# Kernel tuning notes

Measured on AMD Instinct MI355X. Metric: run time of the kernel, lower is better.

## Reference

```python
import jax, jax.numpy as jnp
import numpy as np
import itertools

RADIUS = 0.1
DILATION = 0.05
KSIZE = 3
NDIM = 3
EPS = 1e-12


def _offsets():
    # 3^ndim kernel-cell offsets centered on the particle, spaced by dilation
    half = (KSIZE - 1) / 2.0
    offs = np.array(list(itertools.product(range(KSIZE), repeat=NDIM)), dtype=np.float32)
    return jnp.asarray((offs - half) * DILATION)  # [K, NDIM]


def setup_inputs() -> dict:
    key = jax.random.key(0)
    k1, k2, k3, k4, k5 = jax.random.split(key, 5)
    B, N, C, O = 2, 4096, 16, 16
    K = KSIZE ** NDIM
    locs = jax.random.uniform(k1, (B, N, NDIM), dtype=jnp.float32)
    data = jax.random.normal(k2, (B, N, C), dtype=jnp.float32)
    # densities strictly positive, bounded away from zero
    density = jax.random.uniform(k3, (B, N), dtype=jnp.float32, minval=0.5, maxval=1.5)
    weight = jax.random.normal(k4, (O, C, K), dtype=jnp.float32) * 0.1
    bias = jax.random.normal(k5, (O,), dtype=jnp.float32) * 0.01
    return {"locs": locs, "data": data, "density": density, "weight": weight, "bias": bias}


def reference(locs, data, density, weight, bias):
    # SPH continuous convolution (ConvSP):
    # out[b,i,o] = bias[o] + sum_k sum_c weight[o,c,k] *
    #              sum_j (data[b,j,c]/density[b,j]) * W(||locs[b,j] - (locs[b,i]+off_k)||)
    # with smoothing kernel W(d) = (1 - d/radius)^3 for d < radius, else 0.
    B, N, _ = locs.shape
    O = weight.shape[0]
    offs = _offsets()                                # [K, NDIM]
    wK = jnp.transpose(weight, (2, 0, 1))            # [K, O, C]
    nd = data / density[..., None]                   # [B, N, C] density-normalized features
    l2 = jnp.sum(locs * locs, axis=-1)               # [B, N]

    def step(acc, xs):
        off, wk = xs                                 # off:[NDIM], wk:[O,C]
        c = locs + off                               # shifted query centers [B,N,NDIM]
        c2 = jnp.sum(c * c, axis=-1)                 # [B,N]
        d2 = c2[:, :, None] + l2[:, None, :] - 2.0 * jnp.einsum('bid,bjd->bij', c, locs)
        d = jnp.sqrt(jnp.maximum(d2, EPS))           # [B,N,N]
        w = jnp.where(d < RADIUS, (1.0 - d / RADIUS) ** 3, 0.0)
        kv = jnp.einsum('bij,bjc->bic', w, nd)       # [B,N,C]
        return acc + jnp.einsum('bic,oc->bio', kv, wk), None

    init = jnp.zeros((B, N, O), dtype=data.dtype)
    out, _ = jax.lax.scan(jax.checkpoint(step), init, (offs, wK))
    return out + bias
```

## Files before the change

kernel.cpp:

```cpp
#include <hip/hip_runtime.h>

#define NP 4096
#define NSLAB 64
#define ZSPAN 10
#define EPS_K 1e-12f
#define MAXH 256

__global__ __launch_bounds__(1024) void k_bins(const float* __restrict__ locs,
                                               int* __restrict__ off,
                                               int* __restrict__ cursor) {
    __shared__ int s_cnt[NSLAB];
    const int b = blockIdx.x;
    const int tid = threadIdx.x;
    if (tid < NSLAB) s_cnt[tid] = 0;
    __syncthreads();
    const float* lz = locs + (size_t)b * NP * 3;
    for (int i = tid; i < NP; i += 1024) {
        float z = lz[i * 3 + 2];
        int c = min(max((int)(z * 64.0f), 0), 63);
        atomicAdd(&s_cnt[c], 1);
    }
    __syncthreads();
    if (tid < 64) {
        int incl = s_cnt[tid];
        for (int d = 1; d < 64; d <<= 1) {
            int o = __shfl_up(incl, d, 64);
            if (tid >= d) incl += o;
        }
        off[b * (NSLAB + 1) + tid + 1] = incl;
        if (tid == 0) off[b * (NSLAB + 1)] = 0;
        cursor[b * NSLAB + tid] = 0;
    }
}

__global__ __launch_bounds__(256) void k_scatter(
    const float* __restrict__ locs, const float* __restrict__ data,
    const float* __restrict__ density, const float* __restrict__ weight,
    const int* __restrict__ off, int* __restrict__ cursor,
    float4* __restrict__ slocs, float4* __restrict__ snd, float* __restrict__ wT)
{
    const int tid = threadIdx.x;
    const int b = blockIdx.x >> 4;
    const int il = ((blockIdx.x & 15) << 8) + tid;
    const size_t gi = ((size_t)b << 12) + il;
    const float* lp = locs + gi * 3;
    const float x = lp[0], y = lp[1], z = lp[2];
    const int bin = min(max((int)(z * 64.0f), 0), 63);
    const int r = atomicAdd(&cursor[b * NSLAB + bin], 1);
    const int pos = off[b * (NSLAB + 1) + bin] + r;
    const size_t gp = ((size_t)b << 12) + pos;

    float4 s4 = { x, y, z, __int_as_float(il) };
    slocs[gp] = s4;
    const float invr = 1.0f / density[gi];
    const float4* dsrc = (const float4*)data + (gi << 2);
    float4* ddst = snd + (gp << 2);
#pragma unroll
    for (int q = 0; q < 4; ++q) {
        float4 v = dsrc[q];
        float4 o4 = { v.x * invr, v.y * invr, v.z * invr, v.w * invr };
        ddst[q] = o4;
    }

    if (blockIdx.x == 0) {
        for (int i2 = tid; i2 < 27 * 256; i2 += 256) {
            int k = i2 >> 8, oc = i2 & 255;
            wT[k * 256 + oc] = weight[oc * 27 + k];
        }
    }
}

__global__ __launch_bounds__(256) void k_main(
    const float4* __restrict__ slocs,
    const float4* __restrict__ snd,
    const int* __restrict__ off,
    const float* __restrict__ wT,
    const float* __restrict__ bias,
    float* __restrict__ out)
{
    __shared__ float4 s_hits[4][MAXH];

    const int tid  = threadIdx.x;
    const int wid  = tid >> 6;
    const int lane = tid & 63;
    const int hsh  = lane & 32;
    const int l32  = lane & 31;

    const int bid = blockIdx.x;
    const int b   = bid >> 10;
    const int p   = ((bid & 1023) << 2) + wid;

    const float4* slb  = slocs + ((size_t)b << 12);
    const float4* sndb = snd   + ((size_t)b << 14);
    const int*    offb = off + b * (NSLAB + 1);
    float4* hl = s_hits[wid];

    const float4 me = slb[p];
    const int orig = __float_as_int(me.w);
    const int sp = min(max((int)(me.z * 64.0f), 0), 63);
    const int jstart = offb[max(sp - ZSPAN, 0)];
    const int jend   = offb[min(sp + ZSPAN, NSLAB - 1) + 1];

    float cx, cy, cz;
    {
        int kk = (l32 < 27) ? l32 : 13;
        cx = me.x + (float)(kk / 9       - 1) * 0.05f;
        cy = me.y + (float)((kk / 3) % 3 - 1) * 0.05f;
        cz = me.z + (float)(kk % 3       - 1) * 0.05f;
        if (l32 >= 27) cx = 1e9f;
    }

    int nh = 0;
    const int nsteps = (jend - jstart + 63) >> 6;
    for (int st = 0; st < nsteps; ++st) {
        const int j = jstart + (st << 6) + lane;
        float4 lj = slb[min(j, jend - 1)];
        if (j >= jend) lj.x = 1e9f;
        const float ex = fmaxf(fabsf(me.x - lj.x) - 0.05f, 0.f);
        const float ey = fmaxf(fabsf(me.y - lj.y) - 0.05f, 0.f);
        const float ez = fmaxf(fabsf(me.z - lj.z) - 0.05f, 0.f);
        const float bd2 = ex * ex + ey * ey + ez * ez;
        const bool pred = bd2 < 0.01f;
        const unsigned long long ball = __ballot(pred);
        const int pos = nh + (int)__popcll(ball & ((1ull << lane) - 1ull));
        if (pred && pos < MAXH - 3) {
            float4 rec = { lj.x, lj.y, lj.z, __int_as_float(j) };
            hl[pos] = rec;
        }
        nh += (int)__popcll(ball);
    }
    nh = min(nh, MAXH - 3);
    if (lane < 3) {
        float4 padr = { 1e9f, 1e9f, 1e9f, __int_as_float(0) };
        hl[nh + lane] = padr;
    }

    float kv[16];
#pragma unroll
    for (int c = 0; c < 16; ++c) kv[c] = 0.f;

    const int hoff = hsh >> 5;
    const int nt = (nh + 1) >> 1;
    float4 rec = hl[hoff];
    for (int t = 0; t < nt; ++t) {
        const int j = __float_as_int(rec.w);
        const float4* dp = sndb + ((size_t)j << 2);
        const float4 v0 = dp[0], v1 = dp[1], v2 = dp[2], v3 = dp[3];
        const float4 recn = hl[((t + 1) << 1) + hoff];
        const float dx = cx - rec.x, dy = cy - rec.y, dz = cz - rec.z;
        const float d2 = dx * dx + dy * dy + dz * dz;
        const float d = sqrtf(fmaxf(d2, EPS_K));
        float t1 = fmaxf(__builtin_fmaf(d, -10.f, 1.f), 0.f);
        const float w = t1 * t1 * t1;
        kv[ 0] = fmaf(w, v0.x, kv[ 0]);
        kv[ 1] = fmaf(w, v0.y, kv[ 1]);
        kv[ 2] = fmaf(w, v0.z, kv[ 2]);
        kv[ 3] = fmaf(w, v0.w, kv[ 3]);
        kv[ 4] = fmaf(w, v1.x, kv[ 4]);
        kv[ 5] = fmaf(w, v1.y, kv[ 5]);
        kv[ 6] = fmaf(w, v1.z, kv[ 6]);
        kv[ 7] = fmaf(w, v1.w, kv[ 7]);
        kv[ 8] = fmaf(w, v2.x, kv[ 8]);
        kv[ 9] = fmaf(w, v2.y, kv[ 9]);
        kv[10] = fmaf(w, v2.z, kv[10]);
        kv[11] = fmaf(w, v2.w, kv[11]);
        kv[12] = fmaf(w, v3.x, kv[12]);
        kv[13] = fmaf(w, v3.y, kv[13]);
        kv[14] = fmaf(w, v3.z, kv[14]);
        kv[15] = fmaf(w, v3.w, kv[15]);
        rec = recn;
    }

#pragma unroll
    for (int c = 0; c < 16; ++c)
        kv[c] += __shfl_xor(kv[c], 32, 64);

    const int kk = (l32 < 27) ? l32 : 26;
    const float4* wrow = (const float4*)(wT + kk * 256);
    float res = 0.f;
#pragma unroll
    for (int o = 0; o < 16; ++o) {
        const float4 w0 = wrow[o * 4 + 0], w1 = wrow[o * 4 + 1];
        const float4 w2 = wrow[o * 4 + 2], w3 = wrow[o * 4 + 3];
        float acc = 0.f;
        acc = fmaf(w0.x, kv[ 0], acc); acc = fmaf(w0.y, kv[ 1], acc);
        acc = fmaf(w0.z, kv[ 2], acc); acc = fmaf(w0.w, kv[ 3], acc);
        acc = fmaf(w1.x, kv[ 4], acc); acc = fmaf(w1.y, kv[ 5], acc);
        acc = fmaf(w1.z, kv[ 6], acc); acc = fmaf(w1.w, kv[ 7], acc);
        acc = fmaf(w2.x, kv[ 8], acc); acc = fmaf(w2.y, kv[ 9], acc);
        acc = fmaf(w2.z, kv[10], acc); acc = fmaf(w2.w, kv[11], acc);
        acc = fmaf(w3.x, kv[12], acc); acc = fmaf(w3.y, kv[13], acc);
        acc = fmaf(w3.z, kv[14], acc); acc = fmaf(w3.w, kv[15], acc);
#pragma unroll
        for (int dsh = 16; dsh >= 1; dsh >>= 1)
            acc += __shfl_xor(acc, dsh, 32);
        if (l32 == o) res = acc;
    }
    if (lane < 16)
        out[(((size_t)(b << 12)) + orig) * 16 + lane] = res + bias[lane];
}

extern "C" void kernel_launch(void* const* d_in, const int* in_sizes, int n_in,
                              void* d_out, int out_size, void* d_ws, size_t ws_size,
                              hipStream_t stream) {
    const float* locs    = (const float*)d_in[0];
    const float* data    = (const float*)d_in[1];
    const float* density = (const float*)d_in[2];
    const float* weight  = (const float*)d_in[3];
    const float* bias    = (const float*)d_in[4];
    float* out = (float*)d_out;

    const int B = in_sizes[2] / NP;
    const int totalP = B * NP;

    char* ws = (char*)d_ws;
    size_t o = 0;
    auto take = [&](size_t bytes) { size_t r = o; o = (o + bytes + 255) & ~(size_t)255; return r; };
    float4* slocs  = (float4*)(ws + take((size_t)totalP * 16));
    float4* snd    = (float4*)(ws + take((size_t)totalP * 64));
    float*  wT     = (float*)(ws + take(27 * 256 * 4));
    int*    cursor = (int*)(ws + take((size_t)B * NSLAB * 4));
    int*    off    = (int*)(ws + take((size_t)B * (NSLAB + 1) * 4));

    k_bins<<<B, 1024, 0, stream>>>(locs, off, cursor);
    k_scatter<<<totalP / 256, 256, 0, stream>>>(locs, data, density, weight,
                                                off, cursor, slocs, snd, wT);
    k_main<<<B * 1024, 256, 0, stream>>>(slocs, snd, off, wT, bias, out);
}
```

Measured before the change: 117.9 us.

## Fuse neighbor filtering with accumulation, dropping LDS hit list and splitting output channels

```diff
diff --git a/kernel.cpp b/kernel.cpp
--- a/kernel.cpp
+++ b/kernel.cpp
@@ -4,7 +4,6 @@
 #define NSLAB 64
 #define ZSPAN 10
 #define EPS_K 1e-12f
-#define MAXH 256
 
 __global__ __launch_bounds__(1024) void k_bins(const float* __restrict__ locs,
                                                int* __restrict__ off,
@@ -78,13 +77,12 @@
     const float* __restrict__ bias,
     float* __restrict__ out)
 {
-    __shared__ float4 s_hits[4][MAXH];
-
     const int tid  = threadIdx.x;
     const int wid  = tid >> 6;
     const int lane = tid & 63;
     const int hsh  = lane & 32;
     const int l32  = lane & 31;
+    const int hoff = hsh >> 5;
 
     const int bid = blockIdx.x;
     const int b   = bid >> 10;
@@ -93,7 +91,6 @@
     const float4* slb  = slocs + ((size_t)b << 12);
     const float4* sndb = snd   + ((size_t)b << 14);
     const int*    offb = off + b * (NSLAB + 1);
-    float4* hl = s_hits[wid];
 
     const float4 me = slb[p];
     const int orig = __float_as_int(me.w);
@@ -110,65 +107,68 @@
         if (l32 >= 27) cx = 1e9f;
     }
 
-    int nh = 0;
+    float kv[16];
+#pragma unroll
+    for (int c = 0; c < 16; ++c) kv[c] = 0.f;
+
     const int nsteps = (jend - jstart + 63) >> 6;
+    float4 cur, nxt;
+    {
+        const int j0 = jstart + lane;
+        cur = slb[min(j0, jend - 1)];
+        if (j0 >= jend) cur.x = 1e9f;
+        const int j1 = jstart + 64 + lane;
+        nxt = slb[min(j1, jend - 1)];
+        if (j1 >= jend) nxt.x = 1e9f;
+    }
+
     for (int st = 0; st < nsteps; ++st) {
-        const int j = jstart + (st << 6) + lane;
-        float4 lj = slb[min(j, jend - 1)];
-        if (j >= jend) lj.x = 1e9f;
-        const float ex = fmaxf(fabsf(me.x - lj.x) - 0.05f, 0.f);
-        const float ey = fmaxf(fabsf(me.y - lj.y) - 0.05f, 0.f);
-        const float ez = fmaxf(fabsf(me.z - lj.z) - 0.05f, 0.f);
+        const int tbase = jstart + (st << 6);
+        const int j2 = tbase + 128 + lane;
+        float4 t2 = slb[min(j2, jend - 1)];
+        if (j2 >= jend) t2.x = 1e9f;
+
+        const float ex = fmaxf(fabsf(me.x - cur.x) - 0.05f, 0.f);
+        const float ey = fmaxf(fabsf(me.y - cur.y) - 0.05f, 0.f);
+        const float ez = fmaxf(fabsf(me.z - cur.z) - 0.05f, 0.f);
         const float bd2 = ex * ex + ey * ey + ez * ez;
-        const bool pred = bd2 < 0.01f;
-        const unsigned long long ball = __ballot(pred);
-        const int pos = nh + (int)__popcll(ball & ((1ull << lane) - 1ull));
-        if (pred && pos < MAXH - 3) {
-            float4 rec = { lj.x, lj.y, lj.z, __int_as_float(j) };
-            hl[pos] = rec;
+        const unsigned long long ball = __ballot(bd2 < 0.01f);
+        unsigned int mh = (unsigned int)(ball >> hsh);
+        const int cbase = tbase + hsh;
+
+        while (mh) {
+            const int bit = __ffs(mh) - 1;
+            mh &= mh - 1;
+            const int j = cbase + bit;
+            const float4* dp = sndb + ((size_t)j << 2);
+            const float4 v0 = dp[0], v1 = dp[1], v2 = dp[2], v3 = dp[3];
+            const float qx = __shfl(cur.x, bit, 32);
+            const float qy = __shfl(cur.y, bit, 32);
+            const float qz = __shfl(cur.z, bit, 32);
+            const float dx = cx - qx, dy = cy - qy, dz = cz - qz;
+            const float d2 = dx * dx + dy * dy + dz * dz;
+            const float d = sqrtf(fmaxf(d2, EPS_K));
+            float t1 = fmaxf(__builtin_fmaf(d, -10.f, 1.f), 0.f);
+            const float w = t1 * t1 * t1;
+            kv[ 0] = fmaf(w, v0.x, kv[ 0]);
+            kv[ 1] = fmaf(w, v0.y, kv[ 1]);
+            kv[ 2] = fmaf(w, v0.z, kv[ 2]);
+            kv[ 3] = fmaf(w, v0.w, kv[ 3]);
+            kv[ 4] = fmaf(w, v1.x, kv[ 4]);
+            kv[ 5] = fmaf(w, v1.y, kv[ 5]);
+            kv[ 6] = fmaf(w, v1.z, kv[ 6]);
+            kv[ 7] = fmaf(w, v1.w, kv[ 7]);
+            kv[ 8] = fmaf(w, v2.x, kv[ 8]);
+            kv[ 9] = fmaf(w, v2.y, kv[ 9]);
+            kv[10] = fmaf(w, v2.z, kv[10]);
+            kv[11] = fmaf(w, v2.w, kv[11]);
+            kv[12] = fmaf(w, v3.x, kv[12]);
+            kv[13] = fmaf(w, v3.y, kv[13]);
+            kv[14] = fmaf(w, v3.z, kv[14]);
+            kv[15] = fmaf(w, v3.w, kv[15]);
         }
-        nh += (int)__popcll(ball);
-    }
-    nh = min(nh, MAXH - 3);
-    if (lane < 3) {
-        float4 padr = { 1e9f, 1e9f, 1e9f, __int_as_float(0) };
-        hl[nh + lane] = padr;
-    }
-
-    float kv[16];
-#pragma unroll
-    for (int c = 0; c < 16; ++c) kv[c] = 0.f;
-
-    const int hoff = hsh >> 5;
-    const int nt = (nh + 1) >> 1;
-    float4 rec = hl[hoff];
-    for (int t = 0; t < nt; ++t) {
-        const int j = __float_as_int(rec.w);
-        const float4* dp = sndb + ((size_t)j << 2);
-        const float4 v0 = dp[0], v1 = dp[1], v2 = dp[2], v3 = dp[3];
-        const float4 recn = hl[((t + 1) << 1) + hoff];
-        const float dx = cx - rec.x, dy = cy - rec.y, dz = cz - rec.z;
-        const float d2 = dx * dx + dy * dy + dz * dz;
-        const float d = sqrtf(fmaxf(d2, EPS_K));
-        float t1 = fmaxf(__builtin_fmaf(d, -10.f, 1.f), 0.f);
-        const float w = t1 * t1 * t1;
-        kv[ 0] = fmaf(w, v0.x, kv[ 0]);
-        kv[ 1] = fmaf(w, v0.y, kv[ 1]);
-        kv[ 2] = fmaf(w, v0.z, kv[ 2]);
-        kv[ 3] = fmaf(w, v0.w, kv[ 3]);
-        kv[ 4] = fmaf(w, v1.x, kv[ 4]);
-        kv[ 5] = fmaf(w, v1.y, kv[ 5]);
-        kv[ 6] = fmaf(w, v1.z, kv[ 6]);
-        kv[ 7] = fmaf(w, v1.w, kv[ 7]);
-        kv[ 8] = fmaf(w, v2.x, kv[ 8]);
-        kv[ 9] = fmaf(w, v2.y, kv[ 9]);
-        kv[10] = fmaf(w, v2.z, kv[10]);
-        kv[11] = fmaf(w, v2.w, kv[11]);
-        kv[12] = fmaf(w, v3.x, kv[12]);
-        kv[13] = fmaf(w, v3.y, kv[13]);
-        kv[14] = fmaf(w, v3.z, kv[14]);
-        kv[15] = fmaf(w, v3.w, kv[15]);
-        rec = recn;
+        cur = nxt;
+        nxt = t2;
     }
 
 #pragma unroll
@@ -176,12 +176,12 @@
         kv[c] += __shfl_xor(kv[c], 32, 64);
 
     const int kk = (l32 < 27) ? l32 : 26;
-    const float4* wrow = (const float4*)(wT + kk * 256);
+    const int obase = hoff << 3;
     float res = 0.f;
 #pragma unroll
-    for (int o = 0; o < 16; ++o) {
-        const float4 w0 = wrow[o * 4 + 0], w1 = wrow[o * 4 + 1];
-        const float4 w2 = wrow[o * 4 + 2], w3 = wrow[o * 4 + 3];
+    for (int oo = 0; oo < 8; ++oo) {
+        const float4* wrow = (const float4*)(wT + kk * 256 + (obase + oo) * 16);
+        const float4 w0 = wrow[0], w1 = wrow[1], w2 = wrow[2], w3 = wrow[3];
         float acc = 0.f;
         acc = fmaf(w0.x, kv[ 0], acc); acc = fmaf(w0.y, kv[ 1], acc);
         acc = fmaf(w0.z, kv[ 2], acc); acc = fmaf(w0.w, kv[ 3], acc);
@@ -194,10 +194,10 @@
 #pragma unroll
         for (int dsh = 16; dsh >= 1; dsh >>= 1)
             acc += __shfl_xor(acc, dsh, 32);
-        if (l32 == o) res = acc;
-    }
-    if (lane < 16)
-        out[(((size_t)(b << 12)) + orig) * 16 + lane] = res + bias[lane];
+        if (l32 == oo) res = acc;
+    }
+    if (l32 < 8)
+        out[(((size_t)(b << 12)) + orig) * 16 + obase + l32] = res + bias[obase + l32];
 }
 
 extern "C" void kernel_launch(void* const* d_in, const int* in_sizes, int n_in,
```

Result: faster. 102.7 us (-12.9%).
